# Optimization experiments

Hardware: AMD Instinct MI355X
Metric: run time of the kernel (lower is better)

Reference implementation:

```python
import jax, jax.numpy as jnp
import numpy as np

N_BLOCKS = 100
LAYERS_PER_BLOCK = 10
D = 100
D_OUT = 10
BATCH = 65536


def setup_inputs() -> dict:
    key = jax.random.key(0)
    ks = jax.random.split(key, 6)
    bound = 1.0 / np.sqrt(D)  # PyTorch default Linear init bound
    x = jax.random.normal(ks[0], (BATCH, D), dtype=jnp.float32)
    # Stacked weights: [n_blocks, layers_per_block, out, in]
    W = jax.random.uniform(ks[1], (N_BLOCKS, LAYERS_PER_BLOCK, D, D), jnp.float32, -bound, bound)
    b = jax.random.uniform(ks[2], (N_BLOCKS, LAYERS_PER_BLOCK, D), jnp.float32, -bound, bound)
    Wf = jax.random.uniform(ks[3], (D_OUT, D), jnp.float32, -bound, bound)
    bf = jax.random.uniform(ks[4], (D_OUT,), jnp.float32, -bound, bound)
    return {"x": x, "W": W, "b": b, "Wf": Wf, "bf": bf}


def reference(x, W, b, Wf, bf):
    def layer_step(y, wb):
        w, bb = wb  # w: [D, D] (out, in), bb: [D]
        return jax.nn.relu(y @ w.T + bb), None

    def block_step(xb, wb):
        Wb, bb = wb  # [LAYERS_PER_BLOCK, D, D], [LAYERS_PER_BLOCK, D]
        y, _ = jax.lax.scan(layer_step, xb, (Wb, bb))
        return xb + y, None

    out, _ = jax.lax.scan(block_step, x, (W, b))
    return out @ Wf.T + bf
```

## Files before the change

kernel.cpp:

```cpp
#include <hip/hip_runtime.h>
#include <hip/hip_bf16.h>

#define N_LAYERS 1000
#define DD 100
#define DOUT 10
#define FRAG 4096
#define LSTRIDE (7 * FRAG)
#define POFF_MAX ((size_t)(N_LAYERS * 7 - 1) * FRAG)

typedef short s8v __attribute__((ext_vector_type(8)));
typedef float f16v __attribute__((ext_vector_type(16)));
typedef float f4v __attribute__((ext_vector_type(4)));

__device__ __forceinline__ unsigned short f2bf(float f) {
  __hip_bfloat16 h = __float2bfloat16(f);
  return *reinterpret_cast<unsigned short*>(&h);
}
__device__ __forceinline__ float bf2f(unsigned short h) {
  return __uint_as_float(((unsigned)h) << 16);
}
__device__ __forceinline__ unsigned pk2(float a, float b) {
  return (unsigned)f2bf(a) | ((unsigned)f2bf(b) << 16);
}

__global__ __launch_bounds__(256)
void presplit_kernel(const float* __restrict__ W, const float* __restrict__ b,
                     char* __restrict__ hi_g) {
  int idx = blockIdx.x * 256 + threadIdx.x;
  if (idx >= N_LAYERS * 7 * 4 * 64) return;
  int lane = idx & 63;
  int gf = (idx >> 6) & 3;
  int r = idx >> 8;
  int ks = r % 7;
  int L = r / 7;
  int n = gf * 32 + (lane & 31);
  int k0 = ks * 16 + (lane >> 5) * 8;
  s8v hv;
#pragma unroll
  for (int j = 0; j < 8; ++j) {
    int k = k0 + j;
    float v = 0.0f;
    if (n < DD) {
      if (k < DD) v = W[((size_t)L * DD + n) * DD + k];
      else if (k == DD) v = b[(size_t)L * DD + n];
    }
    hv[j] = (short)f2bf(v);
  }
  *(s8v*)(hi_g + (size_t)idx * 16) = hv;
}

__device__ __forceinline__ void wload_f32(s8v* h, int L, int ks, int l31, int lhi,
                                          const float* __restrict__ W_g,
                                          const float* __restrict__ b_g) {
#pragma unroll
  for (int gf = 0; gf < 4; ++gf) {
    int n = gf * 32 + l31;
    int k0 = ks * 16 + lhi * 8;
    s8v hv;
#pragma unroll
    for (int j = 0; j < 8; ++j) {
      int k = k0 + j;
      float v = 0.0f;
      if (n < DD) {
        if (k < DD) v = W_g[((size_t)L * DD + n) * DD + k];
        else if (k == DD) v = b_g[(size_t)L * DD + n];
      }
      hv[j] = (short)f2bf(v);
    }
    h[gf] = hv;
  }
}

template <int PRE, int LP>
__device__ __forceinline__ void layer_step(
    int L, s8v (&bf)[7], s8v (&wh)[4][4],
    const char* __restrict__ pW, size_t& poff, char* __restrict__ xrb,
    const f16v& zro, const float* __restrict__ W_g, const float* __restrict__ b_g,
    int l31, int lhi) {
  const bool bend = ((L % 10) == 9);
  f16v acc[4];
#pragma unroll
  for (int ks = 0; ks < 7; ++ks) {
    const int s = (3 * LP + ks) & 3;
    if (ks == 0) {
#pragma unroll
      for (int g = 0; g < 4; ++g)
        acc[g] = __builtin_amdgcn_mfma_f32_32x32x16_bf16(wh[s][g], bf[0], zro, 0, 0, 0);
    } else {
#pragma unroll
      for (int g = 0; g < 4; ++g)
        acc[g] = __builtin_amdgcn_mfma_f32_32x32x16_bf16(wh[s][g], bf[ks], acc[g], 0, 0, 0);
    }
    if (PRE) {
      if (poff <= POFF_MAX) {
#pragma unroll
        for (int g = 0; g < 4; ++g)
          wh[s][g] = *(const s8v*)(pW + poff + g * 1024);
      }
      poff += FRAG;
    } else {
      const int Ln = L + (ks >= 3 ? 1 : 0);
      const int nks = (ks + 4) % 7;
      if (Ln < N_LAYERS) wload_f32(wh[s], Ln, nks, l31, lhi, W_g, b_g);
    }
  }

  unsigned P0[4][4], P1[4][4];
#pragma unroll
  for (int g = 0; g < 4; ++g) {
#pragma unroll
    for (int q = 0; q < 4; ++q) {
      float o0 = fmaxf(acc[g][4 * q + 0], 0.0f);
      float o1 = fmaxf(acc[g][4 * q + 1], 0.0f);
      float o2 = fmaxf(acc[g][4 * q + 2], 0.0f);
      float o3 = fmaxf(acc[g][4 * q + 3], 0.0f);
      if (bend) {
        f4v xq = *(const f4v*)(xrb + (g * 4 + q) * 2048);
        o0 += xq[0]; o1 += xq[1]; o2 += xq[2]; o3 += xq[3];
        f4v nv; nv[0] = o0; nv[1] = o1; nv[2] = o2; nv[3] = o3;
        *(f4v*)(xrb + (g * 4 + q) * 2048) = nv;
      }
      P0[g][q] = pk2(o0, o1);
      P1[g][q] = pk2(o2, o3);
    }
  }
#pragma unroll
  for (int ks = 0; ks < 7; ++ks) {
    const int g = ks >> 1;
    const int qa = 2 * (ks & 1);
    auto rA = __builtin_amdgcn_permlane32_swap((int)P0[g][qa], (int)P0[g][qa + 1], false, false);
    auto rB = __builtin_amdgcn_permlane32_swap((int)P1[g][qa], (int)P1[g][qa + 1], false, false);
    union { s8v v; unsigned u[4]; } t;
    t.u[0] = (unsigned)rA[0];
    t.u[1] = (unsigned)rB[0];
    t.u[2] = (ks == 6) ? 0x3F80u : (unsigned)rA[1];
    t.u[3] = (unsigned)rB[1];
    bf[ks] = t.v;
  }
}

template <int PRE>
__global__ __launch_bounds__(128, 2)
void resnet_main(const float* __restrict__ x_g,
                 const float* __restrict__ W_g, const float* __restrict__ b_g,
                 const float* __restrict__ Wf_g, const float* __restrict__ bf_g,
                 float* __restrict__ out_g,
                 const char* __restrict__ whi_g) {
  __shared__ char xs[32768];

  const int tid = threadIdx.x;
  const int lane = tid & 63;
  const int wv = tid >> 6;
  const int l31 = lane & 31;
  const int lhi = lane >> 5;
  const int row = blockIdx.x * 64 + wv * 32 + l31;

  s8v bf[7];
#pragma unroll
  for (int ks = 0; ks < 7; ++ks) {
    const int k0 = ks * 16 + lhi * 8;
    unsigned w[4];
#pragma unroll
    for (int p = 0; p < 4; ++p) {
      const int ka = k0 + 2 * p, kb = k0 + 2 * p + 1;
      float a0 = (ka < DD) ? x_g[(size_t)row * DD + ka] : (ka == DD ? 1.0f : 0.0f);
      float a1 = (kb < DD) ? x_g[(size_t)row * DD + kb] : (kb == DD ? 1.0f : 0.0f);
      w[p] = pk2(a0, a1);
    }
    union { s8v v; unsigned u[4]; } t;
    t.u[0] = w[0]; t.u[1] = w[1]; t.u[2] = w[2]; t.u[3] = w[3];
    bf[ks] = t.v;
  }

  char* xrb = xs + tid * 16;
#pragma unroll
  for (int g = 0; g < 4; ++g) {
#pragma unroll
    for (int q = 0; q < 4; ++q) {
      f4v xq;
#pragma unroll
      for (int j = 0; j < 4; ++j) {
        int c = 32 * g + 8 * q + j + 4 * lhi;
        xq[j] = (c < DD) ? x_g[(size_t)row * DD + c] : 0.0f;
      }
      *(f4v*)(xrb + (g * 4 + q) * 2048) = xq;
    }
  }

  f16v zro;
#pragma unroll
  for (int r = 0; r < 16; ++r) zro[r] = 0.0f;

  const char* pW = whi_g + lane * 16;
  s8v wh[4][4];
  if (PRE) {
#pragma unroll
    for (int s = 0; s < 4; ++s)
#pragma unroll
      for (int g = 0; g < 4; ++g)
        wh[s][g] = *(const s8v*)(pW + s * FRAG + g * 1024);
  } else {
#pragma unroll
    for (int s = 0; s < 4; ++s) wload_f32(wh[s], 0, s, l31, lhi, W_g, b_g);
  }
  size_t poff = 4 * FRAG;

  for (int L = 0; L < N_LAYERS; L += 4) {
    layer_step<PRE, 0>(L + 0, bf, wh, pW, poff, xrb, zro, W_g, b_g, l31, lhi);
    layer_step<PRE, 1>(L + 1, bf, wh, pW, poff, xrb, zro, W_g, b_g, l31, lhi);
    layer_step<PRE, 2>(L + 2, bf, wh, pW, poff, xrb, zro, W_g, b_g, l31, lhi);
    layer_step<PRE, 3>(L + 3, bf, wh, pW, poff, xrb, zro, W_g, b_g, l31, lhi);
  }

  __syncthreads();
  float* xsf = (float*)xs;
  for (int i = tid; i < DOUT * DD; i += 128) xsf[i] = Wf_g[i];
  __syncthreads();

  float part[DOUT];
#pragma unroll
  for (int o = 0; o < DOUT; ++o) part[o] = 0.0f;
#pragma unroll
  for (int ks = 0; ks < 7; ++ks) {
#pragma unroll
    for (int j = 0; j < 8; ++j) {
      const int k = ks * 16 + lhi * 8 + j;
      if (k < DD) {
        float a = bf2f((unsigned short)bf[ks][j]);
#pragma unroll
        for (int o = 0; o < DOUT; ++o) part[o] += a * xsf[o * DD + k];
      }
    }
  }
#pragma unroll
  for (int o = 0; o < DOUT; ++o) part[o] += __shfl_xor(part[o], 32);
  if (lhi == 0) {
#pragma unroll
    for (int o = 0; o < DOUT; ++o)
      out_g[(size_t)row * DOUT + o] = part[o] + bf_g[o];
  }
}

extern "C" void kernel_launch(void* const* d_in, const int* in_sizes, int n_in,
                              void* d_out, int out_size, void* d_ws, size_t ws_size,
                              hipStream_t stream) {
  const float* x = (const float*)d_in[0];
  const float* W = (const float*)d_in[1];
  const float* b = (const float*)d_in[2];
  const float* Wf = (const float*)d_in[3];
  const float* bf = (const float*)d_in[4];
  float* out = (float*)d_out;

  const size_t need = (size_t)N_LAYERS * LSTRIDE;
  const int nwg = 65536 / 64;
  if (ws_size >= need) {
    char* whi = (char*)d_ws;
    const int chunks = N_LAYERS * 7 * 4 * 64;
    presplit_kernel<<<(chunks + 255) / 256, 256, 0, stream>>>(W, b, whi);
    resnet_main<1><<<nwg, 128, 0, stream>>>(x, W, b, Wf, bf, out, whi);
  } else {
    resnet_main<0><<<nwg, 128, 0, stream>>>(x, W, b, Wf, bf, out, nullptr);
  }
}
```

Baseline: 2.087 ms.

## Share layer weights across 4 waves via double-buffered LDS staging

Workgroups grow to 256 threads (4 waves, 128 rows). Each layer's bf16 weights are loaded cooperatively into a double-buffered LDS tile and read by all waves, instead of every wave streaming its own copy of each layer into registers. The residual stream moves from LDS to a global workspace buffer (or to registers in the fallback path). Global weight traffic per row drops, but a __syncthreads is added every layer, LDS reads now sit on the MFMA critical path, and residual updates go through global memory.

```diff
diff --git a/kernel.cpp b/kernel.cpp
--- a/kernel.cpp
+++ b/kernel.cpp
@@ -5,8 +5,8 @@
 #define DD 100
 #define DOUT 10
 #define FRAG 4096
-#define LSTRIDE (7 * FRAG)
-#define POFF_MAX ((size_t)(N_LAYERS * 7 - 1) * FRAG)
+#define LBYTES (7 * FRAG)
+#define NROWS 65536
 
 typedef short s8v __attribute__((ext_vector_type(8)));
 typedef float f16v __attribute__((ext_vector_type(16)));
@@ -49,111 +49,40 @@
   *(s8v*)(hi_g + (size_t)idx * 16) = hv;
 }
 
-__device__ __forceinline__ void wload_f32(s8v* h, int L, int ks, int l31, int lhi,
-                                          const float* __restrict__ W_g,
-                                          const float* __restrict__ b_g) {
-#pragma unroll
-  for (int gf = 0; gf < 4; ++gf) {
-    int n = gf * 32 + l31;
-    int k0 = ks * 16 + lhi * 8;
-    s8v hv;
-#pragma unroll
-    for (int j = 0; j < 8; ++j) {
-      int k = k0 + j;
-      float v = 0.0f;
-      if (n < DD) {
-        if (k < DD) v = W_g[((size_t)L * DD + n) * DD + k];
-        else if (k == DD) v = b_g[(size_t)L * DD + n];
-      }
-      hv[j] = (short)f2bf(v);
-    }
-    h[gf] = hv;
-  }
-}
-
-template <int PRE, int LP>
-__device__ __forceinline__ void layer_step(
-    int L, s8v (&bf)[7], s8v (&wh)[4][4],
-    const char* __restrict__ pW, size_t& poff, char* __restrict__ xrb,
-    const f16v& zro, const float* __restrict__ W_g, const float* __restrict__ b_g,
-    int l31, int lhi) {
-  const bool bend = ((L % 10) == 9);
-  f16v acc[4];
-#pragma unroll
-  for (int ks = 0; ks < 7; ++ks) {
-    const int s = (3 * LP + ks) & 3;
-    if (ks == 0) {
-#pragma unroll
-      for (int g = 0; g < 4; ++g)
-        acc[g] = __builtin_amdgcn_mfma_f32_32x32x16_bf16(wh[s][g], bf[0], zro, 0, 0, 0);
-    } else {
-#pragma unroll
-      for (int g = 0; g < 4; ++g)
-        acc[g] = __builtin_amdgcn_mfma_f32_32x32x16_bf16(wh[s][g], bf[ks], acc[g], 0, 0, 0);
-    }
-    if (PRE) {
-      if (poff <= POFF_MAX) {
-#pragma unroll
-        for (int g = 0; g < 4; ++g)
-          wh[s][g] = *(const s8v*)(pW + poff + g * 1024);
-      }
-      poff += FRAG;
-    } else {
-      const int Ln = L + (ks >= 3 ? 1 : 0);
-      const int nks = (ks + 4) % 7;
-      if (Ln < N_LAYERS) wload_f32(wh[s], Ln, nks, l31, lhi, W_g, b_g);
-    }
-  }
-
-  unsigned P0[4][4], P1[4][4];
-#pragma unroll
-  for (int g = 0; g < 4; ++g) {
-#pragma unroll
-    for (int q = 0; q < 4; ++q) {
-      float o0 = fmaxf(acc[g][4 * q + 0], 0.0f);
-      float o1 = fmaxf(acc[g][4 * q + 1], 0.0f);
-      float o2 = fmaxf(acc[g][4 * q + 2], 0.0f);
-      float o3 = fmaxf(acc[g][4 * q + 3], 0.0f);
-      if (bend) {
-        f4v xq = *(const f4v*)(xrb + (g * 4 + q) * 2048);
-        o0 += xq[0]; o1 += xq[1]; o2 += xq[2]; o3 += xq[3];
-        f4v nv; nv[0] = o0; nv[1] = o1; nv[2] = o2; nv[3] = o3;
-        *(f4v*)(xrb + (g * 4 + q) * 2048) = nv;
-      }
-      P0[g][q] = pk2(o0, o1);
-      P1[g][q] = pk2(o2, o3);
-    }
-  }
-#pragma unroll
-  for (int ks = 0; ks < 7; ++ks) {
-    const int g = ks >> 1;
-    const int qa = 2 * (ks & 1);
-    auto rA = __builtin_amdgcn_permlane32_swap((int)P0[g][qa], (int)P0[g][qa + 1], false, false);
-    auto rB = __builtin_amdgcn_permlane32_swap((int)P1[g][qa], (int)P1[g][qa + 1], false, false);
-    union { s8v v; unsigned u[4]; } t;
-    t.u[0] = (unsigned)rA[0];
-    t.u[1] = (unsigned)rB[0];
-    t.u[2] = (ks == 6) ? 0x3F80u : (unsigned)rA[1];
-    t.u[3] = (unsigned)rB[1];
-    bf[ks] = t.v;
-  }
+__device__ __forceinline__ s8v wconv(int L, int c, int wv, int l31, int lhi,
+                                     const float* __restrict__ W_g,
+                                     const float* __restrict__ b_g) {
+  int n = wv * 32 + l31;
+  int k0 = c * 16 + lhi * 8;
+  s8v hv;
+#pragma unroll
+  for (int j = 0; j < 8; ++j) {
+    int k = k0 + j;
+    float v = 0.0f;
+    if (n < DD) {
+      if (k < DD) v = W_g[((size_t)L * DD + n) * DD + k];
+      else if (k == DD) v = b_g[(size_t)L * DD + n];
+    }
+    hv[j] = (short)f2bf(v);
+  }
+  return hv;
 }
 
 template <int PRE>
-__global__ __launch_bounds__(128, 2)
+__global__ __launch_bounds__(256, 2)
 void resnet_main(const float* __restrict__ x_g,
                  const float* __restrict__ W_g, const float* __restrict__ b_g,
                  const float* __restrict__ Wf_g, const float* __restrict__ bf_g,
                  float* __restrict__ out_g,
-                 const char* __restrict__ whi_g) {
-  __shared__ char xs[32768];
+                 const char* __restrict__ whi_g, char* __restrict__ xr_g) {
+  __shared__ char wbuf[2 * LBYTES];
 
   const int tid = threadIdx.x;
   const int lane = tid & 63;
   const int wv = tid >> 6;
   const int l31 = lane & 31;
   const int lhi = lane >> 5;
-  const int row = blockIdx.x * 64 + wv * 32 + l31;
+  const int row = blockIdx.x * 128 + wv * 32 + l31;
 
   s8v bf[7];
 #pragma unroll
@@ -172,49 +101,129 @@
     bf[ks] = t.v;
   }
 
-  char* xrb = xs + tid * 16;
-#pragma unroll
-  for (int g = 0; g < 4; ++g) {
-#pragma unroll
-    for (int q = 0; q < 4; ++q) {
+  f4v xrr[13];
+#pragma unroll
+  for (int q16 = 0; q16 <= 12; ++q16) {
+    const int c0 = 32 * (q16 >> 2) + 8 * (q16 & 3) + 4 * lhi;
+    if (c0 < DD) {
       f4v xq;
 #pragma unroll
       for (int j = 0; j < 4; ++j) {
-        int c = 32 * g + 8 * q + j + 4 * lhi;
+        int c = c0 + j;
         xq[j] = (c < DD) ? x_g[(size_t)row * DD + c] : 0.0f;
       }
-      *(f4v*)(xrb + (g * 4 + q) * 2048) = xq;
-    }
-  }
+      if (PRE) *(f4v*)(xr_g + ((size_t)(q16 * 2 + lhi) * NROWS + row) * 16) = xq;
+      else xrr[q16] = xq;
+    }
+  }
+
+#pragma unroll
+  for (int c = 0; c < 7; ++c) {
+    s8v v;
+    if (PRE) v = *(const s8v*)(whi_g + c * FRAG + tid * 16);
+    else     v = wconv(0, c, wv, l31, lhi, W_g, b_g);
+    *(s8v*)(&wbuf[c * FRAG + tid * 16]) = v;
+  }
+  __syncthreads();
 
   f16v zro;
 #pragma unroll
   for (int r = 0; r < 16; ++r) zro[r] = 0.0f;
 
-  const char* pW = whi_g + lane * 16;
-  s8v wh[4][4];
-  if (PRE) {
-#pragma unroll
-    for (int s = 0; s < 4; ++s)
-#pragma unroll
-      for (int g = 0; g < 4; ++g)
-        wh[s][g] = *(const s8v*)(pW + s * FRAG + g * 1024);
-  } else {
-#pragma unroll
-    for (int s = 0; s < 4; ++s) wload_f32(wh[s], 0, s, l31, lhi, W_g, b_g);
-  }
-  size_t poff = 4 * FRAG;
-
-  for (int L = 0; L < N_LAYERS; L += 4) {
-    layer_step<PRE, 0>(L + 0, bf, wh, pW, poff, xrb, zro, W_g, b_g, l31, lhi);
-    layer_step<PRE, 1>(L + 1, bf, wh, pW, poff, xrb, zro, W_g, b_g, l31, lhi);
-    layer_step<PRE, 2>(L + 2, bf, wh, pW, poff, xrb, zro, W_g, b_g, l31, lhi);
-    layer_step<PRE, 3>(L + 3, bf, wh, pW, poff, xrb, zro, W_g, b_g, l31, lhi);
+  int cur = 0;
+  for (int L = 0; L < N_LAYERS; ++L) {
+    const bool more = (L + 1 < N_LAYERS);
+
+    s8v stg[7];
+    if (more) {
+      if (PRE) {
+        const char* ps = whi_g + (size_t)(L + 1) * LBYTES + tid * 16;
+#pragma unroll
+        for (int c = 0; c < 7; ++c) stg[c] = *(const s8v*)(ps + c * FRAG);
+      } else {
+#pragma unroll
+        for (int c = 0; c < 7; ++c) stg[c] = wconv(L + 1, c, wv, l31, lhi, W_g, b_g);
+      }
+    }
+
+    const char* rb = &wbuf[cur * LBYTES] + lane * 16;
+    s8v wr[2][4];
+#pragma unroll
+    for (int g = 0; g < 4; ++g) wr[0][g] = *(const s8v*)(rb + g * 1024);
+    f16v acc[4];
+#pragma unroll
+    for (int ks = 0; ks < 7; ++ks) {
+      const int s = ks & 1;
+      if (ks < 6) {
+#pragma unroll
+        for (int g = 0; g < 4; ++g)
+          wr[s ^ 1][g] = *(const s8v*)(rb + (ks + 1) * FRAG + g * 1024);
+      }
+      if (ks == 0) {
+#pragma unroll
+        for (int g = 0; g < 4; ++g)
+          acc[g] = __builtin_amdgcn_mfma_f32_32x32x16_bf16(wr[0][g], bf[0], zro, 0, 0, 0);
+      } else {
+#pragma unroll
+        for (int g = 0; g < 4; ++g)
+          acc[g] = __builtin_amdgcn_mfma_f32_32x32x16_bf16(wr[s][g], bf[ks], acc[g], 0, 0, 0);
+      }
+    }
+
+    const bool bend = ((L % 10) == 9);
+#pragma unroll
+    for (int ks = 0; ks < 7; ++ks) {
+      const int g = ks >> 1, qa = 2 * (ks & 1);
+      unsigned pa[2], pb[2];
+#pragma unroll
+      for (int t = 0; t < 2; ++t) {
+        const int q = qa + t;
+        float o0 = fmaxf(acc[g][4 * q + 0], 0.0f);
+        float o1 = fmaxf(acc[g][4 * q + 1], 0.0f);
+        float o2 = fmaxf(acc[g][4 * q + 2], 0.0f);
+        float o3 = fmaxf(acc[g][4 * q + 3], 0.0f);
+        if (bend) {
+          const int q16 = g * 4 + q;
+          const int c0 = 32 * g + 8 * q + 4 * lhi;
+          if (c0 < DD) {
+            if (PRE) {
+              char* xp = xr_g + ((size_t)(q16 * 2 + lhi) * NROWS + row) * 16;
+              f4v xq = *(const f4v*)xp;
+              o0 += xq[0]; o1 += xq[1]; o2 += xq[2]; o3 += xq[3];
+              f4v nv; nv[0] = o0; nv[1] = o1; nv[2] = o2; nv[3] = o3;
+              *(f4v*)xp = nv;
+            } else {
+              f4v xq = xrr[q16];
+              o0 += xq[0]; o1 += xq[1]; o2 += xq[2]; o3 += xq[3];
+              f4v nv; nv[0] = o0; nv[1] = o1; nv[2] = o2; nv[3] = o3;
+              xrr[q16] = nv;
+            }
+          }
+        }
+        pa[t] = pk2(o0, o1); pb[t] = pk2(o2, o3);
+      }
+      auto rA = __builtin_amdgcn_permlane32_swap((int)pa[0], (int)pa[1], false, false);
+      auto rB = __builtin_amdgcn_permlane32_swap((int)pb[0], (int)pb[1], false, false);
+      union { s8v v; unsigned u[4]; } t2;
+      t2.u[0] = (unsigned)rA[0];
+      t2.u[1] = (unsigned)rB[0];
+      t2.u[2] = (ks == 6) ? 0x3F80u : (unsigned)rA[1];
+      t2.u[3] = (unsigned)rB[1];
+      bf[ks] = t2.v;
+    }
+
+    if (more) {
+      char* wd = &wbuf[(cur ^ 1) * LBYTES] + tid * 16;
+#pragma unroll
+      for (int c = 0; c < 7; ++c) *(s8v*)(wd + c * FRAG) = stg[c];
+    }
+    __syncthreads();
+    cur ^= 1;
   }
 
   __syncthreads();
-  float* xsf = (float*)xs;
-  for (int i = tid; i < DOUT * DD; i += 128) xsf[i] = Wf_g[i];
+  float* xsf = (float*)wbuf;
+  for (int i = tid; i < DOUT * DD; i += 256) xsf[i] = Wf_g[i];
   __syncthreads();
 
   float part[DOUT];
@@ -251,14 +260,17 @@
   const float* bf = (const float*)d_in[4];
   float* out = (float*)d_out;
 
-  const size_t need = (size_t)N_LAYERS * LSTRIDE;
-  const int nwg = 65536 / 64;
+  const size_t wpack = (size_t)N_LAYERS * LBYTES;
+  const size_t xrbytes = (size_t)25 * NROWS * 16;
+  const size_t need = wpack + xrbytes;
+  const int nwg = 65536 / 128;
   if (ws_size >= need) {
     char* whi = (char*)d_ws;
+    char* xr = whi + wpack;
     const int chunks = N_LAYERS * 7 * 4 * 64;
     presplit_kernel<<<(chunks + 255) / 256, 256, 0, stream>>>(W, b, whi);
-    resnet_main<1><<<nwg, 128, 0, stream>>>(x, W, b, Wf, bf, out, whi);
+    resnet_main<1><<<nwg, 256, 0, stream>>>(x, W, b, Wf, bf, out, whi, xr);
   } else {
-    resnet_main<0><<<nwg, 128, 0, stream>>>(x, W, b, Wf, bf, out, nullptr);
-  }
-}
+    resnet_main<0><<<nwg, 256, 0, stream>>>(x, W, b, Wf, bf, out, nullptr, nullptr);
+  }
+}
```

New measurement: 2.163 ms. 1.04x slower.
